# Kernel optimization log

Measured on AMD Instinct MI355X. Metric: run time of the kernel, lower is better.

The kernel has to match this reference:

```python
import jax, jax.numpy as jnp
import numpy as np

N = 100000      # nodes
E = 800000      # edges
F_IN = 128      # input feature dim
HID = 32        # GAT out_channels per head
H = 4           # heads
HC = HID * H    # 128, concat width (== F_IN by design)
EDIM = 16       # raw edge feature dim
G = 256         # number of graphs in batch
OUT = 2         # output classes
SLOPE = 0.2     # GATConv LeakyReLU negative slope
BN_EPS = 1e-5


def setup_inputs() -> dict:
    key = jax.random.key(0)
    ks = jax.random.split(key, 16)
    s = 0.05
    x = jax.random.normal(ks[0], (N, F_IN), jnp.float32)
    edge_index = jax.random.randint(ks[1], (2, E), 0, N, dtype=jnp.int64)
    edge_attr = jax.random.normal(ks[2], (E, EDIM), jnp.float32)
    batch = jnp.sort(jax.random.randint(ks[3], (N,), 0, G, dtype=jnp.int64))
    edge_fc_W = jax.random.normal(ks[4], (EDIM, HID), jnp.float32) * s
    edge_fc_b = jnp.zeros((HID,), jnp.float32)
    # all 3 GAT layers have in_dim 128 -> H*C 128, so stack them
    Ws = jax.random.normal(ks[5], (3, F_IN, HC), jnp.float32) * s
    att_src = jax.random.normal(ks[6], (3, H, HID), jnp.float32) * s
    att_dst = jax.random.normal(ks[7], (3, H, HID), jnp.float32) * s
    att_edge = jax.random.normal(ks[8], (3, H, HID), jnp.float32) * s
    lin_e = jax.random.normal(ks[9], (3, HID, HC), jnp.float32) * s
    biases = jnp.zeros((3, HC), jnp.float32)
    bn_gamma = jnp.ones((3, HC), jnp.float32)
    bn_beta = jnp.zeros((3, HC), jnp.float32)
    fc_W = jax.random.normal(ks[10], (HC, OUT), jnp.float32) * s
    fc_b = jnp.zeros((OUT,), jnp.float32)
    return {"x": x, "edge_index": edge_index, "edge_attr": edge_attr, "batch": batch,
            "edge_fc_W": edge_fc_W, "edge_fc_b": edge_fc_b, "Ws": Ws,
            "att_src": att_src, "att_dst": att_dst, "att_edge": att_edge,
            "lin_e": lin_e, "biases": biases, "bn_gamma": bn_gamma,
            "bn_beta": bn_beta, "fc_W": fc_W, "fc_b": fc_b}


def _gat_layer(h, e_h, src, dst, W, a_s, a_d, a_e, We, b):
    xl = (h @ W).reshape(N, H, HID)            # [N,H,C]
    el = (e_h @ We).reshape(E, H, HID)         # [E,H,C]
    alpha = ((xl * a_s).sum(-1)[src]           # alpha_src gathered at source
             + (xl * a_d).sum(-1)[dst]         # alpha_dst gathered at target
             + (el * a_e).sum(-1))             # [E,H]
    alpha = jax.nn.leaky_relu(alpha, SLOPE)
    # segment softmax over incoming edges of each destination node
    amax = jax.ops.segment_max(alpha, dst, num_segments=N)
    ealpha = jnp.exp(alpha - amax[dst])
    denom = jax.ops.segment_sum(ealpha, dst, num_segments=N)
    alpha = ealpha / (denom[dst] + 1e-16)
    # weighted scatter-aggregate of source messages
    out = jax.ops.segment_sum(alpha[:, :, None] * xl[src], dst, num_segments=N)
    return out.reshape(N, HC) + b


def reference(x, edge_index, edge_attr, batch, edge_fc_W, edge_fc_b, Ws,
              att_src, att_dst, att_edge, lin_e, biases, bn_gamma, bn_beta,
              fc_W, fc_b):
    src, dst = edge_index[0], edge_index[1]
    e_h = edge_attr @ edge_fc_W + edge_fc_b   # [E, HID]
    h = x
    for l in range(3):
        h = _gat_layer(h, e_h, src, dst, Ws[l], att_src[l], att_dst[l],
                       att_edge[l], lin_e[l], biases[l])
        # BatchNorm1d over node dim (training-mode batch statistics)
        mu = h.mean(0)
        var = h.var(0)
        h = (h - mu) * jax.lax.rsqrt(var + BN_EPS) * bn_gamma[l] + bn_beta[l]
        h = jax.nn.relu(h)
        # dropout_rate = 0.0 -> identity
    # global mean pool per graph
    sums = jax.ops.segment_sum(h, batch, num_segments=G)
    cnt = jax.ops.segment_sum(jnp.ones((N,), h.dtype), batch, num_segments=G)
    pooled = sums / jnp.maximum(cnt, 1.0)[:, None]   # [G, HC]
    return pooled @ fc_W + fc_b                      # [G, OUT]
```

## Files before the change

### kernel.cpp

```cpp
#include <hip/hip_runtime.h>

#define Nn 100000
#define Ee 800000
#define HC 128
#define HID 32
#define NHD 4
#define EDIM 16
#define Gg 256
#define NOUT 2
#define SLOPE 0.2f
#define BN_EPS 1e-5f
#define SCHUNK 1024
#define NSB 98
#define NBAG 6250

typedef unsigned int u32;
typedef unsigned short u16;
typedef short v8s __attribute__((ext_vector_type(8)));
typedef float v4f __attribute__((ext_vector_type(4)));

union PkAB { u32 u[4]; v8s v; };

__device__ __forceinline__ float bflo(u32 u){ return __uint_as_float(u << 16); }
__device__ __forceinline__ float bfhi(u32 u){ return __uint_as_float(u & 0xFFFF0000u); }

__device__ __forceinline__ u32 bf16rne(float x)
{
  u32 b = __float_as_uint(x);
  return (b + 0x7FFFu + ((b >> 16) & 1u)) >> 16;
}
__device__ __forceinline__ u32 packsplit(float x)
{
  u32 hb = bf16rne(x);
  float hf = __uint_as_float(hb << 16);
  u32 lb = bf16rne(x - hf);
  return hb | (lb << 16);
}
__device__ __forceinline__ void split2(float f, u32& hb, u32& lb)
{
  hb = bf16rne(f);
  lb = bf16rne(f - __uint_as_float(hb << 16));
}

__global__ void compute_K(const float* __restrict__ efcW, const float* __restrict__ efcb,
                          const float* __restrict__ linE, const float* __restrict__ attE,
                          float* __restrict__ Kmat, float* __restrict__ kb)
{
  __shared__ float Msh[384];
  int t = threadIdx.x;
  if (t < 384) {
    int l = t >> 7, j = (t >> 2) & 31, h = t & 3;
    float m = 0.f;
    for (int c = 0; c < 32; ++c)
      m += linE[(l*32 + j)*128 + h*32 + c] * attE[(l*4 + h)*32 + c];
    Msh[l*128 + j*4 + h] = m;
  }
  __syncthreads();
  if (t < 192) {
    int k = t / 12, col = t % 12, l = col >> 2, h = col & 3;
    float acc = 0.f;
    for (int j = 0; j < 32; ++j)
      acc += efcW[k*32 + j] * Msh[l*128 + j*4 + h];
    Kmat[k*12 + col] = acc;
  } else if (t < 204) {
    int col = t - 192, l = col >> 2, h = col & 3;
    float acc = 0.f;
    for (int j = 0; j < 32; ++j)
      acc += efcb[j] * Msh[l*128 + j*4 + h];
    kb[col] = acc;
  }
}

__global__ void w_split(const float* __restrict__ Wall, u32* __restrict__ Wf)
{
  int tid = blockIdx.x * 256 + threadIdx.x;
  if (tid >= 3*HC*HC) return;
  int l = tid / (HC*HC);
  int rem = tid - l*HC*HC;
  int k = rem >> 7, n = rem & 127;
  u32 p = packsplit(Wall[tid]);
  int nt = n >> 4, col = n & 15;
  int ks = k >> 5, kin = k & 31, q = kin >> 3, j = kin & 7;
  int half = j >> 2, j4 = j & 3;
  int idx = ((((l*8 + nt)*4 + ks)*2 + half)*64 + q*16 + col)*4 + j4;
  Wf[idx] = p;
}

__global__ void k_hist(const int* __restrict__ dst, int* __restrict__ deg)
{
  int e = blockIdx.x * 256 + threadIdx.x;
  if (e < Ee) atomicAdd(&deg[dst[e]], 1);
}

__global__ void k_bsum(const int* __restrict__ deg, int* __restrict__ bsum)
{
  __shared__ int sh[256];
  int b = blockIdx.x, t = threadIdx.x;
  int s = 0;
  for (int i = t; i < SCHUNK; i += 256) {
    int idx = b*SCHUNK + i;
    if (idx < Nn) s += deg[idx];
  }
  sh[t] = s; __syncthreads();
  for (int o = 128; o; o >>= 1) { if (t < o) sh[t] += sh[t+o]; __syncthreads(); }
  if (!t) bsum[b] = sh[0];
}

__global__ void k_mid(const int* __restrict__ bsum, int* __restrict__ bpre, int* __restrict__ rowp)
{
  __shared__ int sh[NSB];
  int t = threadIdx.x;
  if (t < NSB) sh[t] = bsum[t];
  __syncthreads();
  if (!t) {
    int run = 0;
    for (int i = 0; i < NSB; ++i) { int v = sh[i]; sh[i] = run; run += v; }
    rowp[Nn] = run;
  }
  __syncthreads();
  if (t < NSB) bpre[t] = sh[t];
}

__global__ void k_scan(const int* __restrict__ deg, const int* __restrict__ bpre, int* __restrict__ rowp)
{
  __shared__ int sh[SCHUNK];
  int b = blockIdx.x, t = threadIdx.x;
  for (int i = t; i < SCHUNK; i += 256) {
    int idx = b*SCHUNK + i;
    sh[i] = (idx < Nn) ? deg[idx] : 0;
  }
  __syncthreads();
  if (!t) {
    int run = 0;
    for (int i = 0; i < SCHUNK; ++i) { int v = sh[i]; sh[i] = run; run += v; }
  }
  __syncthreads();
  int base = bpre[b];
  for (int i = t; i < SCHUNK; i += 256) {
    int idx = b*SCHUNK + i;
    if (idx < Nn) rowp[idx] = sh[i] + base;
  }
}

__global__ void k_fillpre(const int* __restrict__ src, const int* __restrict__ dst,
                          const float* __restrict__ eattr,
                          const float* __restrict__ Kmat, const float* __restrict__ kb,
                          const int* __restrict__ rowp, int* __restrict__ fill,
                          u32* __restrict__ rec)
{
  int e = blockIdx.x * 256 + threadIdx.x;
  if (e >= Ee) return;
  const float4* p = (const float4*)(eattr + (size_t)e * EDIM);
  float ea[16];
  #pragma unroll
  for (int qq = 0; qq < 4; ++qq) {
    float4 v = p[qq];
    ea[qq*4+0] = v.x; ea[qq*4+1] = v.y; ea[qq*4+2] = v.z; ea[qq*4+3] = v.w;
  }
  float ep[12];
  #pragma unroll
  for (int col = 0; col < 12; ++col) ep[col] = kb[col];
  #pragma unroll
  for (int k = 0; k < 16; ++k) {
    float v = ea[k];
    #pragma unroll
    for (int col = 0; col < 12; ++col) ep[col] += v * Kmat[k*12 + col];
  }
  int d = dst[e];
  int pos = rowp[d] + atomicAdd(&fill[d], 1);
  uint4 r0, r1;
  r0.x = bf16rne(ep[0])  | (bf16rne(ep[1])  << 16);
  r0.y = bf16rne(ep[2])  | (bf16rne(ep[3])  << 16);
  r0.z = bf16rne(ep[4])  | (bf16rne(ep[5])  << 16);
  r0.w = bf16rne(ep[6])  | (bf16rne(ep[7])  << 16);
  r1.x = bf16rne(ep[8])  | (bf16rne(ep[9])  << 16);
  r1.y = bf16rne(ep[10]) | (bf16rne(ep[11]) << 16);
  r1.z = (u32)src[e];
  r1.w = 0;
  uint4* rp = (uint4*)(rec + (size_t)pos * 8);
  rp[0] = r0; rp[1] = r1;
}

__device__ __forceinline__ int lbound(const int* __restrict__ a, int n, int key)
{
  int lo = 0, hi = n;
  while (lo < hi) {
    int mid = (lo + hi) >> 1;
    if (a[mid] < key) lo = mid + 1; else hi = mid;
  }
  return lo;
}

__global__ void k_gb(const int* __restrict__ batch, int* __restrict__ gb)
{
  int g = blockIdx.x * 256 + threadIdx.x;
  if (g <= Gg) gb[g] = lbound(batch, Nn, g);
}

__global__ void split_x(const float* __restrict__ src, u32* __restrict__ dst)
{
  int idx = blockIdx.x * 256 + threadIdx.x;
  if (idx >= Nn*HC/4) return;
  float4 v = ((const float4*)src)[idx];
  uint4 o;
  o.x = packsplit(v.x); o.y = packsplit(v.y);
  o.z = packsplit(v.z); o.w = packsplit(v.w);
  ((uint4*)dst)[idx] = o;
}

__global__ __launch_bounds__(256, 4) void gemm_mfma(const u32* __restrict__ Apk,
                                                    const u32* __restrict__ Wf,
                                                    u16* __restrict__ C2,
                                                    const float* __restrict__ aS,
                                                    const float* __restrict__ aD,
                                                    float* __restrict__ as_,
                                                    float* __restrict__ ad_,
                                                    const float* __restrict__ scb,
                                                    const float* __restrict__ shb,
                                                    int apply_bn)
{
  __shared__ uint4 Bsh[1024];
  int t = threadIdx.x;
  int w = t >> 6, lane = t & 63;
  int col = lane & 15, q = lane >> 4;
  int rbase = blockIdx.x * 64 + w * 16;

  v4f acc[8];
  #pragma unroll
  for (int nt = 0; nt < 8; ++nt) acc[nt] = (v4f){0.f, 0.f, 0.f, 0.f};

  const uint4* Wf4 = (const uint4*)Wf;

  int ar = rbase + col;
  if (ar >= Nn) ar = Nn - 1;
  const uint4* pa = (const uint4*)(Apk + (size_t)ar*HC);
  uint4 ra[8];
  #pragma unroll
  for (int ks = 0; ks < 4; ++ks) {
    ra[2*ks]   = pa[ks*8 + q*2];
    ra[2*ks+1] = pa[ks*8 + q*2 + 1];
  }

  for (int ks = 0; ks < 4; ++ks) {
    #pragma unroll
    for (int i = 0; i < 4; ++i) {
      int u = t + i*256;
      int nt = u >> 7, rem = u & 127;
      Bsh[u] = Wf4[((nt*4 + ks)*2 + (rem >> 6))*64 + (rem & 63)];
    }
    __syncthreads();

    PkAB Ah, Al;
    int cb = ks*32 + q*8;
    uint4 r0 = ra[2*ks], r1 = ra[2*ks+1];
    if (!apply_bn) {
      Ah.u[0] = (r0.x & 0xFFFFu) | (r0.y << 16);
      Al.u[0] = (r0.x >> 16)     | (r0.y & 0xFFFF0000u);
      Ah.u[1] = (r0.z & 0xFFFFu) | (r0.w << 16);
      Al.u[1] = (r0.z >> 16)     | (r0.w & 0xFFFF0000u);
      Ah.u[2] = (r1.x & 0xFFFFu) | (r1.y << 16);
      Al.u[2] = (r1.x >> 16)     | (r1.y & 0xFFFF0000u);
      Ah.u[3] = (r1.z & 0xFFFFu) | (r1.w << 16);
      Al.u[3] = (r1.z >> 16)     | (r1.w & 0xFFFF0000u);
    } else {
      float4 sc0 = *(const float4*)(scb + cb), sc1 = *(const float4*)(scb + cb + 4);
      float4 sh0 = *(const float4*)(shb + cb), sh1 = *(const float4*)(shb + cb + 4);
      float f0 = fmaxf((bflo(r0.x)+bfhi(r0.x))*sc0.x + sh0.x, 0.f);
      float f1 = fmaxf((bflo(r0.y)+bfhi(r0.y))*sc0.y + sh0.y, 0.f);
      float f2 = fmaxf((bflo(r0.z)+bfhi(r0.z))*sc0.z + sh0.z, 0.f);
      float f3 = fmaxf((bflo(r0.w)+bfhi(r0.w))*sc0.w + sh0.w, 0.f);
      float f4 = fmaxf((bflo(r1.x)+bfhi(r1.x))*sc1.x + sh1.x, 0.f);
      float f5 = fmaxf((bflo(r1.y)+bfhi(r1.y))*sc1.y + sh1.y, 0.f);
      float f6 = fmaxf((bflo(r1.z)+bfhi(r1.z))*sc1.z + sh1.z, 0.f);
      float f7 = fmaxf((bflo(r1.w)+bfhi(r1.w))*sc1.w + sh1.w, 0.f);
      u32 hb0,lb0,hb1,lb1,hb2,lb2,hb3,lb3,hb4,lb4,hb5,lb5,hb6,lb6,hb7,lb7;
      split2(f0,hb0,lb0); split2(f1,hb1,lb1); split2(f2,hb2,lb2); split2(f3,hb3,lb3);
      split2(f4,hb4,lb4); split2(f5,hb5,lb5); split2(f6,hb6,lb6); split2(f7,hb7,lb7);
      Ah.u[0] = hb0 | (hb1 << 16);  Al.u[0] = lb0 | (lb1 << 16);
      Ah.u[1] = hb2 | (hb3 << 16);  Al.u[1] = lb2 | (lb3 << 16);
      Ah.u[2] = hb4 | (hb5 << 16);  Al.u[2] = lb4 | (lb5 << 16);
      Ah.u[3] = hb6 | (hb7 << 16);  Al.u[3] = lb6 | (lb7 << 16);
    }
    #pragma unroll
    for (int nt = 0; nt < 8; ++nt) {
      uint4 b0 = Bsh[nt*128 + lane];
      uint4 b1 = Bsh[nt*128 + 64 + lane];
      PkAB Bh, Bl;
      Bh.u[0] = (b0.x & 0xFFFFu) | (b0.y << 16);
      Bl.u[0] = (b0.x >> 16)     | (b0.y & 0xFFFF0000u);
      Bh.u[1] = (b0.z & 0xFFFFu) | (b0.w << 16);
      Bl.u[1] = (b0.z >> 16)     | (b0.w & 0xFFFF0000u);
      Bh.u[2] = (b1.x & 0xFFFFu) | (b1.y << 16);
      Bl.u[2] = (b1.x >> 16)     | (b1.y & 0xFFFF0000u);
      Bh.u[3] = (b1.z & 0xFFFFu) | (b1.w << 16);
      Bl.u[3] = (b1.z >> 16)     | (b1.w & 0xFFFF0000u);
      acc[nt] = __builtin_amdgcn_mfma_f32_16x16x32_bf16(Ah.v, Bh.v, acc[nt], 0, 0, 0);
      acc[nt] = __builtin_amdgcn_mfma_f32_16x16x32_bf16(Ah.v, Bl.v, acc[nt], 0, 0, 0);
      acc[nt] = __builtin_amdgcn_mfma_f32_16x16x32_bf16(Al.v, Bh.v, acc[nt], 0, 0, 0);
    }
    __syncthreads();
  }

  #pragma unroll
  for (int reg = 0; reg < 4; ++reg) {
    int row = rbase + q*4 + reg;
    if (row < Nn) {
      #pragma unroll
      for (int nt = 0; nt < 8; ++nt)
        C2[(size_t)row*HC + nt*16 + col] = (u16)bf16rne(acc[nt][reg]);
    }
  }

  #pragma unroll
  for (int h = 0; h < 4; ++h) {
    float a0 = aS[32*h + col], a1 = aS[32*h + 16 + col];
    float d0 = aD[32*h + col], d1 = aD[32*h + 16 + col];
    #pragma unroll
    for (int reg = 0; reg < 4; ++reg) {
      float s1 = acc[2*h][reg]*a0 + acc[2*h+1][reg]*a1;
      float s2 = acc[2*h][reg]*d0 + acc[2*h+1][reg]*d1;
      s1 += __shfl_xor(s1, 1); s1 += __shfl_xor(s1, 2);
      s1 += __shfl_xor(s1, 4); s1 += __shfl_xor(s1, 8);
      s2 += __shfl_xor(s2, 1); s2 += __shfl_xor(s2, 2);
      s2 += __shfl_xor(s2, 4); s2 += __shfl_xor(s2, 8);
      if (col == 0) {
        int row = rbase + q*4 + reg;
        if (row < Nn) {
          as_[row*NHD + h] = s1;
          ad_[row*NHD + h] = s2;
        }
      }
    }
  }
}

__global__ __launch_bounds__(256) void aggregate(const int* __restrict__ rowp, const u32* __restrict__ rec,
                                                 const float* __restrict__ as_, const float* __restrict__ ad_,
                                                 int l, const u32* __restrict__ xl2,
                                                 const float* __restrict__ bias, u32* __restrict__ outp,
                                                 float* __restrict__ psum, float* __restrict__ psq)
{
  __shared__ float4 rsA[256], rsB[256], rqA[256], rqB[256];
  int t = threadIdx.x;
  int n = blockIdx.x * 16 + (t >> 4);
  int c8 = t & 15;
  int h = c8 >> 2;
  float o[8];
  #pragma unroll
  for (int k = 0; k < 8; ++k) o[k] = 0.f;
  if (n < Nn) {
    int idx = l*4 + h;
    int p = idx >> 1, sel = idx & 1;
    float adh = ad_[n*NHD + h];
    int beg = rowp[n], end = rowp[n+1];
    float acc[8];
    #pragma unroll
    for (int k = 0; k < 8; ++k) acc[k] = 0.f;
    float wsum = 0.f;
    int i = beg;
    for (; i + 8 <= end; i += 8) {
      u32 eu[8]; int s[8]; float av[8]; uint4 v[8];
      #pragma unroll
      for (int j = 0; j < 8; ++j) eu[j] = rec[(size_t)(i+j)*8 + p];
      #pragma unroll
      for (int j = 0; j < 8; ++j) s[j] = (int)rec[(size_t)(i+j)*8 + 6];
      #pragma unroll
      for (int j = 0; j < 8; ++j) av[j] = as_[s[j]*NHD + h];
      #pragma unroll
      for (int j = 0; j < 8; ++j) v[j] = *(const uint4*)(xl2 + (size_t)s[j] * 64 + c8*4);
      #pragma unroll
      for (int j = 0; j < 8; ++j) {
        float ep = sel ? bfhi(eu[j]) : bflo(eu[j]);
        float a = ep + av[j] + adh;
        a = (a > 0.f) ? a : SLOPE * a;
        float wj = __expf(a);
        acc[0] += wj*bflo(v[j].x); acc[1] += wj*bfhi(v[j].x);
        acc[2] += wj*bflo(v[j].y); acc[3] += wj*bfhi(v[j].y);
        acc[4] += wj*bflo(v[j].z); acc[5] += wj*bfhi(v[j].z);
        acc[6] += wj*bflo(v[j].w); acc[7] += wj*bfhi(v[j].w);
        wsum += wj;
      }
    }
    for (; i + 4 <= end; i += 4) {
      u32 eu[4]; int s[4]; float av[4]; uint4 v[4];
      #pragma unroll
      for (int j = 0; j < 4; ++j) eu[j] = rec[(size_t)(i+j)*8 + p];
      #pragma unroll
      for (int j = 0; j < 4; ++j) s[j] = (int)rec[(size_t)(i+j)*8 + 6];
      #pragma unroll
      for (int j = 0; j < 4; ++j) av[j] = as_[s[j]*NHD + h];
      #pragma unroll
      for (int j = 0; j < 4; ++j) v[j] = *(const uint4*)(xl2 + (size_t)s[j] * 64 + c8*4);
      #pragma unroll
      for (int j = 0; j < 4; ++j) {
        float ep = sel ? bfhi(eu[j]) : bflo(eu[j]);
        float a = ep + av[j] + adh;
        a = (a > 0.f) ? a : SLOPE * a;
        float wj = __expf(a);
        acc[0] += wj*bflo(v[j].x); acc[1] += wj*bfhi(v[j].x);
        acc[2] += wj*bflo(v[j].y); acc[3] += wj*bfhi(v[j].y);
        acc[4] += wj*bflo(v[j].z); acc[5] += wj*bfhi(v[j].z);
        acc[6] += wj*bflo(v[j].w); acc[7] += wj*bfhi(v[j].w);
        wsum += wj;
      }
    }
    for (; i < end; ++i) {
      u32 eu = rec[(size_t)i*8 + p];
      int s = (int)rec[(size_t)i*8 + 6];
      float ep = sel ? bfhi(eu) : bflo(eu);
      float a = ep + as_[s*NHD + h] + adh;
      a = (a > 0.f) ? a : SLOPE * a;
      float wj = __expf(a);
      uint4 v = *(const uint4*)(xl2 + (size_t)s * 64 + c8*4);
      acc[0] += wj*bflo(v.x); acc[1] += wj*bfhi(v.x);
      acc[2] += wj*bflo(v.y); acc[3] += wj*bfhi(v.y);
      acc[4] += wj*bflo(v.z); acc[5] += wj*bfhi(v.z);
      acc[6] += wj*bflo(v.w); acc[7] += wj*bfhi(v.w);
      wsum += wj;
    }
    float inv = 1.f / (wsum + 1e-16f);
    uint4 w0, w1;
    #pragma unroll
    for (int k = 0; k < 8; ++k) o[k] = acc[k]*inv + bias[c8*8 + k];
    w0.x = packsplit(o[0]); w0.y = packsplit(o[1]);
    w0.z = packsplit(o[2]); w0.w = packsplit(o[3]);
    w1.x = packsplit(o[4]); w1.y = packsplit(o[5]);
    w1.z = packsplit(o[6]); w1.w = packsplit(o[7]);
    uint4* op = (uint4*)(outp + (size_t)n * HC + c8*8);
    op[0] = w0; op[1] = w1;
  }
  rsA[t] = make_float4(o[0], o[1], o[2], o[3]);
  rsB[t] = make_float4(o[4], o[5], o[6], o[7]);
  rqA[t] = make_float4(o[0]*o[0], o[1]*o[1], o[2]*o[2], o[3]*o[3]);
  rqB[t] = make_float4(o[4]*o[4], o[5]*o[5], o[6]*o[6], o[7]*o[7]);
  __syncthreads();
  for (int off = 128; off >= 16; off >>= 1) {
    if (t < off) {
      rsA[t].x += rsA[t+off].x; rsA[t].y += rsA[t+off].y;
      rsA[t].z += rsA[t+off].z; rsA[t].w += rsA[t+off].w;
      rsB[t].x += rsB[t+off].x; rsB[t].y += rsB[t+off].y;
      rsB[t].z += rsB[t+off].z; rsB[t].w += rsB[t+off].w;
      rqA[t].x += rqA[t+off].x; rqA[t].y += rqA[t+off].y;
      rqA[t].z += rqA[t+off].z; rqA[t].w += rqA[t+off].w;
      rqB[t].x += rqB[t+off].x; rqB[t].y += rqB[t+off].y;
      rqB[t].z += rqB[t+off].z; rqB[t].w += rqB[t+off].w;
    }
    __syncthreads();
  }
  if (t < 16) {
    float4* ps = (float4*)(psum + (size_t)blockIdx.x*HC + t*8);
    ps[0] = rsA[t]; ps[1] = rsB[t];
    float4* pq = (float4*)(psq + (size_t)blockIdx.x*HC + t*8);
    pq[0] = rqA[t]; pq[1] = rqB[t];
  }
}

__global__ __launch_bounds__(256) void k_bnpart(const float* __restrict__ psum, const float* __restrict__ psq,
                                                float* __restrict__ gsum, float* __restrict__ gsq)
{
  __shared__ float4 rs[256], rq[256];
  int t = threadIdx.x;
  int c4 = t & 31, rg = t >> 5;
  float4 s = make_float4(0.f,0.f,0.f,0.f), q = make_float4(0.f,0.f,0.f,0.f);
  for (int k = blockIdx.x*8 + rg; k < NBAG; k += 64*8) {
    float4 a = *(const float4*)(psum + (size_t)k*HC + c4*4);
    float4 b = *(const float4*)(psq  + (size_t)k*HC + c4*4);
    s.x += a.x; s.y += a.y; s.z += a.z; s.w += a.w;
    q.x += b.x; q.y += b.y; q.z += b.z; q.w += b.w;
  }
  rs[t] = s; rq[t] = q;
  __syncthreads();
  for (int off = 128; off >= 32; off >>= 1) {
    if (t < off) {
      rs[t].x += rs[t+off].x; rs[t].y += rs[t+off].y;
      rs[t].z += rs[t+off].z; rs[t].w += rs[t+off].w;
      rq[t].x += rq[t+off].x; rq[t].y += rq[t+off].y;
      rq[t].z += rq[t+off].z; rq[t].w += rq[t+off].w;
    }
    __syncthreads();
  }
  if (t < 32) {
    atomicAdd(&gsum[t*4+0], rs[t].x); atomicAdd(&gsum[t*4+1], rs[t].y);
    atomicAdd(&gsum[t*4+2], rs[t].z); atomicAdd(&gsum[t*4+3], rs[t].w);
    atomicAdd(&gsq[t*4+0], rq[t].x);  atomicAdd(&gsq[t*4+1], rq[t].y);
    atomicAdd(&gsq[t*4+2], rq[t].z);  atomicAdd(&gsq[t*4+3], rq[t].w);
  }
}

__global__ void k_bnfin(float* __restrict__ gsum, float* __restrict__ gsq,
                        const float* __restrict__ gammaL, const float* __restrict__ betaL,
                        float* __restrict__ scb, float* __restrict__ shb)
{
  int c = threadIdx.x;
  float s = gsum[c], q = gsq[c];
  float mu  = s * (1.f / Nn);
  float var = q * (1.f / Nn) - mu * mu;
  float sc = rsqrtf(var + BN_EPS) * gammaL[c];
  scb[c] = sc;
  shb[c] = betaL[c] - mu * sc;
  gsum[c] = 0.f; gsq[c] = 0.f;
}

__global__ __launch_bounds__(256) void pool2(const u32* __restrict__ Ap, const int* __restrict__ gb,
                                             const float* __restrict__ scb, const float* __restrict__ shb,
                                             float* __restrict__ pool)
{
  __shared__ float4 red[256];
  int g = blockIdx.x >> 2, qt = blockIdx.x & 3;
  int t = threadIdx.x;
  int cg = t & 7;
  int rs = t >> 3;
  int c4 = qt*8 + cg;
  int c = c4 * 4;
  int lo = gb[g], hi = gb[g+1];
  float4 s4 = *(const float4*)(scb + c);
  float4 t4 = *(const float4*)(shb + c);
  float4 acc = make_float4(0.f,0.f,0.f,0.f);
  for (int n = lo + rs; n < hi; n += 32) {
    uint4 v = *(const uint4*)(Ap + (size_t)n*HC + c);
    acc.x += fmaxf((bflo(v.x)+bfhi(v.x))*s4.x + t4.x, 0.f);
    acc.y += fmaxf((bflo(v.y)+bfhi(v.y))*s4.y + t4.y, 0.f);
    acc.z += fmaxf((bflo(v.z)+bfhi(v.z))*s4.z + t4.z, 0.f);
    acc.w += fmaxf((bflo(v.w)+bfhi(v.w))*s4.w + t4.w, 0.f);
  }
  red[t] = acc;
  __syncthreads();
  for (int off = 128; off >= 8; off >>= 1) {
    if (t < off) {
      red[t].x += red[t+off].x; red[t].y += red[t+off].y;
      red[t].z += red[t+off].z; red[t].w += red[t+off].w;
    }
    __syncthreads();
  }
  if (t < 8) {
    float inv = 1.f / fmaxf((float)(hi - lo), 1.f);
    float4 r = red[t];
    r.x *= inv; r.y *= inv; r.z *= inv; r.w *= inv;
    *(float4*)(pool + (size_t)g*HC + qt*32 + t*4) = r;
  }
}

__global__ void final_fc(const float* __restrict__ pool,
                         const float* __restrict__ fcW, const float* __restrict__ fcb,
                         float* __restrict__ out)
{
  int t = blockIdx.x * 256 + threadIdx.x;
  if (t >= Gg * NOUT) return;
  int g = t >> 1, o = t & 1;
  float acc = 0.f;
  for (int k = 0; k < HC; ++k)
    acc += pool[(size_t)g * HC + k] * fcW[k * NOUT + o];
  out[t] = acc + fcb[o];
}

extern "C" void kernel_launch(void* const* d_in, const int* in_sizes, int n_in,
                              void* d_out, int out_size, void* d_ws, size_t ws_size,
                              hipStream_t stream)
{
  const float* x      = (const float*)d_in[0];
  const int*   eidx   = (const int*)d_in[1];
  const float* eattr  = (const float*)d_in[2];
  const int*   batch  = (const int*)d_in[3];
  const float* efcW   = (const float*)d_in[4];
  const float* efcb   = (const float*)d_in[5];
  const float* Wall   = (const float*)d_in[6];
  const float* attS   = (const float*)d_in[7];
  const float* attD   = (const float*)d_in[8];
  const float* attE   = (const float*)d_in[9];
  const float* linE   = (const float*)d_in[10];
  const float* biases = (const float*)d_in[11];
  const float* gamma  = (const float*)d_in[12];
  const float* beta   = (const float*)d_in[13];
  const float* fcW    = (const float*)d_in[14];
  const float* fcb    = (const float*)d_in[15];
  float* out = (float*)d_out;

  const int* src = eidx;
  const int* dst = eidx + Ee;

  float* ws    = (float*)d_ws;
  float* bufA  = ws;
  float* bufB  = bufA + (size_t)Nn*HC;
  float* as_   = bufB + (size_t)Nn*HC;
  float* ad_   = as_ + (size_t)Nn*NHD;
  float* Kmat  = ad_ + (size_t)Nn*NHD;
  float* kb    = Kmat + 192;
  float* scb   = kb + 16;
  float* shb   = scb + 128;
  float* gsum  = shb + 128;
  float* gsq   = gsum + 128;
  float* pool  = gsq + 128;
  u32*   rec   = (u32*)(pool + (size_t)Gg*HC);
  u32*   Wf    = rec + (size_t)Ee*8;
  float* psum  = (float*)(Wf + 3*HC*HC);
  float* psq   = psum + (size_t)NBAG*HC;
  int*   gb    = (int*)(psq + (size_t)NBAG*HC);
  int*   rowp  = gb + (Gg + 3);
  int*   deg   = rowp + (Nn + 1);
  int*   fill  = deg + Nn;
  int*   bsum  = fill + Nn;
  int*   bpre  = bsum + 128;

  w_split<<<(3*HC*HC + 255)/256, 256, 0, stream>>>(Wall, Wf);
  compute_K<<<1, 512, 0, stream>>>(efcW, efcb, linE, attE, Kmat, kb);
  k_gb<<<2, 256, 0, stream>>>(batch, gb);

  hipMemsetAsync(deg, 0, 2*Nn*sizeof(int), stream);
  hipMemsetAsync(gsum, 0, 256*sizeof(float), stream);
  k_hist<<<(Ee + 255)/256, 256, 0, stream>>>(dst, deg);
  k_bsum<<<NSB, 256, 0, stream>>>(deg, bsum);
  k_mid<<<1, 128, 0, stream>>>(bsum, bpre, rowp);
  k_scan<<<NSB, 256, 0, stream>>>(deg, bpre, rowp);
  k_fillpre<<<(Ee + 255)/256, 256, 0, stream>>>(src, dst, eattr, Kmat, kb, rowp, fill, rec);

  split_x<<<(Nn*HC/4 + 255)/256, 256, 0, stream>>>(x, (u32*)bufA);

  for (int l = 0; l < 3; ++l) {
    gemm_mfma<<<(Nn + 63)/64, 256, 0, stream>>>((const u32*)bufA, Wf + (size_t)l*HC*HC, (u16*)bufB,
                                                attS + l*HC, attD + l*HC, as_, ad_,
                                                scb, shb, (l > 0) ? 1 : 0);
    aggregate<<<NBAG, 256, 0, stream>>>(rowp, rec, as_, ad_, l, (const u32*)bufB,
                                        biases + l*HC, (u32*)bufA, psum, psq);
    k_bnpart<<<64, 256, 0, stream>>>(psum, psq, gsum, gsq);
    k_bnfin<<<1, 128, 0, stream>>>(gsum, gsq, gamma + l*HC, beta + l*HC, scb, shb);
  }

  pool2<<<Gg*4, 256, 0, stream>>>((const u32*)bufA, gb, scb, shb, pool);
  final_fc<<<2, 256, 0, stream>>>(pool, fcW, fcb, out);
}
```

Before: 610.5 us.

## Split edge records into SoA per-layer arrays and separate permutation pass

Replaces the 32-byte per-edge record (all layers' edge logits plus source index) with a separate source-index array and per-layer 8-byte edge-logit arrays. The per-layer aggregate kernel then reads only 12 bytes per edge instead of touching a 32-byte record, which cuts wasted memory traffic in the three aggregation passes. Building the CSR now takes two kernels: one writes an (edge, src) permutation into the psum scratch buffer, and a second computes the projections in sorted order with coalesced writes. The cost is an extra launch and reading edge attributes in scattered order.

```diff
diff --git a/kernel.cpp b/kernel.cpp
--- a/kernel.cpp
+++ b/kernel.cpp
@@ -142,14 +142,26 @@
   }
 }
 
-__global__ void k_fillpre(const int* __restrict__ src, const int* __restrict__ dst,
-                          const float* __restrict__ eattr,
-                          const float* __restrict__ Kmat, const float* __restrict__ kb,
-                          const int* __restrict__ rowp, int* __restrict__ fill,
-                          u32* __restrict__ rec)
+__global__ void k_mkperm(const int* __restrict__ src, const int* __restrict__ dst,
+                         const int* __restrict__ rowp, int* __restrict__ fill,
+                         uint2* __restrict__ eord)
 {
   int e = blockIdx.x * 256 + threadIdx.x;
   if (e >= Ee) return;
+  int d = dst[e];
+  int pos = rowp[d] + atomicAdd(&fill[d], 1);
+  eord[pos] = make_uint2((u32)e, (u32)src[e]);
+}
+
+__global__ void k_fillpre2(const uint2* __restrict__ eord, const float* __restrict__ eattr,
+                           const float* __restrict__ Kmat, const float* __restrict__ kb,
+                           u32* __restrict__ recS, uint2* __restrict__ recE)
+{
+  int pos = blockIdx.x * 256 + threadIdx.x;
+  if (pos >= Ee) return;
+  uint2 es = eord[pos];
+  int e = (int)es.x;
+  recS[pos] = es.y;
   const float4* p = (const float4*)(eattr + (size_t)e * EDIM);
   float ea[16];
   #pragma unroll
@@ -166,19 +178,13 @@
     #pragma unroll
     for (int col = 0; col < 12; ++col) ep[col] += v * Kmat[k*12 + col];
   }
-  int d = dst[e];
-  int pos = rowp[d] + atomicAdd(&fill[d], 1);
-  uint4 r0, r1;
-  r0.x = bf16rne(ep[0])  | (bf16rne(ep[1])  << 16);
-  r0.y = bf16rne(ep[2])  | (bf16rne(ep[3])  << 16);
-  r0.z = bf16rne(ep[4])  | (bf16rne(ep[5])  << 16);
-  r0.w = bf16rne(ep[6])  | (bf16rne(ep[7])  << 16);
-  r1.x = bf16rne(ep[8])  | (bf16rne(ep[9])  << 16);
-  r1.y = bf16rne(ep[10]) | (bf16rne(ep[11]) << 16);
-  r1.z = (u32)src[e];
-  r1.w = 0;
-  uint4* rp = (uint4*)(rec + (size_t)pos * 8);
-  rp[0] = r0; rp[1] = r1;
+  #pragma unroll
+  for (int l = 0; l < 3; ++l) {
+    uint2 w;
+    w.x = bf16rne(ep[4*l+0]) | (bf16rne(ep[4*l+1]) << 16);
+    w.y = bf16rne(ep[4*l+2]) | (bf16rne(ep[4*l+3]) << 16);
+    recE[(size_t)l*Ee + pos] = w;
+  }
 }
 
 __device__ __forceinline__ int lbound(const int* __restrict__ a, int n, int key)
@@ -334,7 +340,9 @@
   }
 }
 
-__global__ __launch_bounds__(256) void aggregate(const int* __restrict__ rowp, const u32* __restrict__ rec,
+__global__ __launch_bounds__(256) void aggregate(const int* __restrict__ rowp,
+                                                 const u32* __restrict__ recS,
+                                                 const u32* __restrict__ recE,
                                                  const float* __restrict__ as_, const float* __restrict__ ad_,
                                                  int l, const u32* __restrict__ xl2,
                                                  const float* __restrict__ bias, u32* __restrict__ outp,
@@ -349,8 +357,8 @@
   #pragma unroll
   for (int k = 0; k < 8; ++k) o[k] = 0.f;
   if (n < Nn) {
-    int idx = l*4 + h;
-    int p = idx >> 1, sel = idx & 1;
+    const u32* recEl = recE + (size_t)l * ((size_t)Ee * 2);
+    int ph = h >> 1, sel = h & 1;
     float adh = ad_[n*NHD + h];
     int beg = rowp[n], end = rowp[n+1];
     float acc[8];
@@ -361,9 +369,9 @@
     for (; i + 8 <= end; i += 8) {
       u32 eu[8]; int s[8]; float av[8]; uint4 v[8];
       #pragma unroll
-      for (int j = 0; j < 8; ++j) eu[j] = rec[(size_t)(i+j)*8 + p];
-      #pragma unroll
-      for (int j = 0; j < 8; ++j) s[j] = (int)rec[(size_t)(i+j)*8 + 6];
+      for (int j = 0; j < 8; ++j) eu[j] = recEl[(size_t)(i+j)*2 + ph];
+      #pragma unroll
+      for (int j = 0; j < 8; ++j) s[j] = (int)recS[i+j];
       #pragma unroll
       for (int j = 0; j < 8; ++j) av[j] = as_[s[j]*NHD + h];
       #pragma unroll
@@ -384,9 +392,9 @@
     for (; i + 4 <= end; i += 4) {
       u32 eu[4]; int s[4]; float av[4]; uint4 v[4];
       #pragma unroll
-      for (int j = 0; j < 4; ++j) eu[j] = rec[(size_t)(i+j)*8 + p];
-      #pragma unroll
-      for (int j = 0; j < 4; ++j) s[j] = (int)rec[(size_t)(i+j)*8 + 6];
+      for (int j = 0; j < 4; ++j) eu[j] = recEl[(size_t)(i+j)*2 + ph];
+      #pragma unroll
+      for (int j = 0; j < 4; ++j) s[j] = (int)recS[i+j];
       #pragma unroll
       for (int j = 0; j < 4; ++j) av[j] = as_[s[j]*NHD + h];
       #pragma unroll
@@ -405,8 +413,8 @@
       }
     }
     for (; i < end; ++i) {
-      u32 eu = rec[(size_t)i*8 + p];
-      int s = (int)rec[(size_t)i*8 + 6];
+      u32 eu = recEl[(size_t)i*2 + ph];
+      int s = (int)recS[i];
       float ep = sel ? bfhi(eu) : bflo(eu);
       float a = ep + as_[s*NHD + h] + adh;
       a = (a > 0.f) ? a : SLOPE * a;
@@ -591,6 +599,8 @@
   float* gsq   = gsum + 128;
   float* pool  = gsq + 128;
   u32*   rec   = (u32*)(pool + (size_t)Gg*HC);
+  u32*   recS  = rec;
+  u32*   recE  = rec + (size_t)Ee;
   u32*   Wf    = rec + (size_t)Ee*8;
   float* psum  = (float*)(Wf + 3*HC*HC);
   float* psq   = psum + (size_t)NBAG*HC;
@@ -600,6 +610,7 @@
   int*   fill  = deg + Nn;
   int*   bsum  = fill + Nn;
   int*   bpre  = bsum + 128;
+  uint2* eord  = (uint2*)psum;
 
   w_split<<<(3*HC*HC + 255)/256, 256, 0, stream>>>(Wall, Wf);
   compute_K<<<1, 512, 0, stream>>>(efcW, efcb, linE, attE, Kmat, kb);
@@ -611,7 +622,8 @@
   k_bsum<<<NSB, 256, 0, stream>>>(deg, bsum);
   k_mid<<<1, 128, 0, stream>>>(bsum, bpre, rowp);
   k_scan<<<NSB, 256, 0, stream>>>(deg, bpre, rowp);
-  k_fillpre<<<(Ee + 255)/256, 256, 0, stream>>>(src, dst, eattr, Kmat, kb, rowp, fill, rec);
+  k_mkperm<<<(Ee + 255)/256, 256, 0, stream>>>(src, dst, rowp, fill, eord);
+  k_fillpre2<<<(Ee + 255)/256, 256, 0, stream>>>(eord, eattr, Kmat, kb, recS, (uint2*)recE);
 
   split_x<<<(Nn*HC/4 + 255)/256, 256, 0, stream>>>(x, (u32*)bufA);
 
@@ -619,7 +631,7 @@
     gemm_mfma<<<(Nn + 63)/64, 256, 0, stream>>>((const u32*)bufA, Wf + (size_t)l*HC*HC, (u16*)bufB,
                                                 attS + l*HC, attD + l*HC, as_, ad_,
                                                 scb, shb, (l > 0) ? 1 : 0);
-    aggregate<<<NBAG, 256, 0, stream>>>(rowp, rec, as_, ad_, l, (const u32*)bufB,
+    aggregate<<<NBAG, 256, 0, stream>>>(rowp, recS, recE, as_, ad_, l, (const u32*)bufB,
                                         biases + l*HC, (u32*)bufA, psum, psq);
     k_bnpart<<<64, 256, 0, stream>>>(psum, psq, gsum, gsq);
     k_bnfin<<<1, 128, 0, stream>>>(gsum, gsq, gamma + l*HC, beta + l*HC, scb, shb);
```

Measured after the change: 622.2 us. No clear change (+1.9%).
